# Performance work log

Measured on AMD Instinct MI355X. Metric: run time of the kernel, lower is better.

The kernel has to match this reference:

```python
import jax, jax.numpy as jnp
import numpy as np

B, T_IMG, H, W_ = 8, 64, 112, 112
T_Q, QDIM, D, NH, HD = 4096, 242, 512, 8, 64
MAX_KV = 512
NUM_CLASSES = 1296
F_IN = 3 * H * W_


def _ln(x, g, b, eps=1e-5):
    m = x.mean(-1, keepdims=True)
    v = ((x - m) ** 2).mean(-1, keepdims=True)
    return (x - m) * jax.lax.rsqrt(v + eps) * g + b


def _pool_mean(x, lengths, max_kv):
    # x: (B, T, D); per-row stride s = ceil(L / max_kv); pooled[j] = mean of window of size s
    # (zero-padded past L, divided by s), matching torch _pool_variable_1d(mode='mean').
    Bx, T, Dx = x.shape
    s = jnp.maximum((lengths + max_kv - 1) // max_kv, 1)          # (B,)
    S = -(-T // max_kv)                                            # static max stride
    j = jnp.arange(max_kv)
    i = jnp.arange(S)
    idx = j[None, :, None] * s[:, None, None] + i[None, None, :]   # (B, max_kv, S)
    valid = (i[None, None, :] < s[:, None, None]) & (idx < lengths[:, None, None])
    gi = jnp.minimum(idx, T - 1).reshape(Bx, -1)[:, :, None]       # (B, max_kv*S, 1)
    g = jnp.take_along_axis(x, gi, axis=1).reshape(Bx, max_kv, S, Dx)
    pooled = (g * valid[..., None].astype(x.dtype)).sum(2) / s[:, None, None].astype(x.dtype)
    new_len = (lengths + s - 1) // s                               # ceil(L/s) <= max_kv
    pad_mask = jnp.arange(max_kv)[None, :] >= new_len[:, None]     # True = PAD
    pooled = jnp.where(pad_mask[..., None], jnp.zeros((), x.dtype), pooled)
    return pooled, new_len, pad_mask


def setup_inputs() -> dict:
    key = jax.random.key(0)
    ks = jax.random.split(key, 20)
    sc = lambda n: np.float32(1.0 / np.sqrt(n))
    d = {}
    d["images"] = jax.random.normal(ks[0], (B, T_IMG, 3, H, W_), jnp.float32)
    d["qgrids"] = jax.random.normal(ks[1], (B, T_Q, QDIM), jnp.float32)
    d["keypoints"] = jax.random.normal(ks[2], (B, T_IMG, QDIM), jnp.float32)
    d["qgrid_lengths"] = jax.random.randint(ks[3], (B,), 512, T_Q + 1)
    d["W_img"] = jax.random.normal(ks[4], (F_IN, D), jnp.float32) * sc(F_IN)
    d["b_img"] = jnp.zeros((D,), jnp.float32)
    d["W_kp"] = jax.random.normal(ks[5], (QDIM, D), jnp.float32) * sc(QDIM)
    d["b_kp"] = jnp.zeros((D,), jnp.float32)
    d["g_kp"] = jnp.ones((D,), jnp.float32)
    d["bt_kp"] = jnp.zeros((D,), jnp.float32)
    d["W_qp"] = jax.random.normal(ks[6], (QDIM, D), jnp.float32) * sc(QDIM)
    d["b_qp"] = jnp.zeros((D,), jnp.float32)
    d["g_qln"] = jnp.ones((D,), jnp.float32)
    d["bt_qln"] = jnp.zeros((D,), jnp.float32)
    d["Wq"] = jax.random.normal(ks[7], (D, D), jnp.float32) * sc(D)
    d["bq"] = jnp.zeros((D,), jnp.float32)
    d["Wk"] = jax.random.normal(ks[8], (D, D), jnp.float32) * sc(D)
    d["bk"] = jnp.zeros((D,), jnp.float32)
    d["Wv"] = jax.random.normal(ks[9], (D, D), jnp.float32) * sc(D)
    d["bv"] = jnp.zeros((D,), jnp.float32)
    d["Wo"] = jax.random.normal(ks[10], (D, D), jnp.float32) * sc(D)
    d["bo"] = jnp.zeros((D,), jnp.float32)
    d["g_attn"] = jnp.ones((D,), jnp.float32)
    d["bt_attn"] = jnp.zeros((D,), jnp.float32)
    d["W_ctc"] = jax.random.normal(ks[11], (2 * D, NUM_CLASSES), jnp.float32) * sc(2 * D)
    d["b_ctc"] = jnp.zeros((NUM_CLASSES,), jnp.float32)
    return d


def reference(images, qgrids, keypoints, qgrid_lengths, W_img, b_img, W_kp, b_kp,
              g_kp, bt_kp, W_qp, b_qp, g_qln, bt_qln, Wq, bq, Wk, bk, Wv, bv,
              Wo, bo, g_attn, bt_attn, W_ctc, b_ctc):
    Bx, T = images.shape[:2]
    # image encoder stub: per-frame flatten -> linear -> (B, T, D)
    img_feat = images.reshape(Bx, T, -1) @ W_img + b_img
    kp_feat = _ln(jax.nn.relu(keypoints @ W_kp + b_kp), g_kp, bt_kp)
    low = img_feat + kp_feat                                       # (B, T_img, D)
    # qgrid proj + LN, then ragged variable-stride mean pooling to <= MAX_KV tokens
    q_emb = _ln(qgrids @ W_qp + b_qp, g_qln, bt_qln)               # (B, T_q, D)
    q_emb, q_lens, pad = _pool_mean(q_emb, qgrid_lengths, MAX_KV)  # (B, MAX_KV, D)
    # cross attention: queries = low-freq frames, keys/values = pooled qgrid tokens
    q = (low @ Wq + bq).reshape(Bx, T, NH, HD)
    k = (q_emb @ Wk + bk).reshape(Bx, MAX_KV, NH, HD)
    v = (q_emb @ Wv + bv).reshape(Bx, MAX_KV, NH, HD)
    scores = jnp.einsum('bqhd,bkhd->bhqk', q, k) * (1.0 / np.sqrt(HD))
    scores = jnp.where(pad[:, None, None, :], jnp.asarray(-1e9, scores.dtype), scores)
    attn = jax.nn.softmax(scores, axis=-1)
    ctx = jnp.einsum('bhqk,bkhd->bqhd', attn, v).reshape(Bx, T, D)
    ctx = _ln(ctx @ Wo + bo, g_attn, bt_attn)
    fused = jnp.concatenate([low, ctx], axis=-1)                   # (B, T_img, 2D)
    return fused @ W_ctc + b_ctc                                   # (B, T_img, V)
```

## Files before the change

### kernel.cpp

```cpp
#include <hip/hip_runtime.h>
#include <hip/hip_bf16.h>

typedef __bf16 bf16x8 __attribute__((ext_vector_type(8)));
typedef __bf16 bf16x4 __attribute__((ext_vector_type(4)));
typedef float f32x4 __attribute__((ext_vector_type(4)));
typedef float f32x2 __attribute__((ext_vector_type(2)));

__device__ __forceinline__ f32x4 mfma16(bf16x8 a, bf16x8 b, f32x4 c) {
  return __builtin_amdgcn_mfma_f32_16x16x32_bf16(a, b, c, 0, 0, 0);
}

__device__ __forceinline__ bf16x8 cvt8(const float* f) {
  bf16x8 r;
#pragma unroll
  for (int i = 0; i < 8; ++i) r[i] = (__bf16)f[i];
  return r;
}

#define SYNC_LGKM() \
  asm volatile("s_waitcnt lgkmcnt(0)\n\ts_barrier" ::: "memory")

__device__ __forceinline__ void blockRed2(float& a, float& b, float* red) {
#pragma unroll
  for (int off = 1; off < 64; off <<= 1) {
    a += __shfl_xor(a, off, 64);
    b += __shfl_xor(b, off, 64);
  }
  const int w = threadIdx.x >> 6;
  if ((threadIdx.x & 63) == 0) { red[w] = a; red[4 + w] = b; }
  __syncthreads();
  a = red[0] + red[1] + red[2] + red[3];
  b = red[4] + red[5] + red[6] + red[7];
  __syncthreads();
}

#define IMG_K 37632
#define SPLITK 49
#define STEPS_PER 24

__global__ __launch_bounds__(512) void img_gemm_kernel(
    const float* __restrict__ A, const float* __restrict__ B,
    __bf16* __restrict__ partials) {
  __shared__ __bf16 As[2][128 * 40];
  __shared__ __bf16 Bs[2][128 * 40];
  const int t = threadIdx.x;
  const int lane = t & 63;
  const int w = t >> 6;
  const int wr = (w >> 2) * 64;
  const int wc = (w & 3) * 32;
  const int orig = blockIdx.x + (blockIdx.y << 2) + (blockIdx.z << 4);
  const int swz = (orig & 7) * 98 + (orig >> 3);
  const int m0 = ((swz >> 2) & 3) * 128;
  const int n0 = (swz & 3) * 128;
  const int zz = swz >> 4;
  const int step0 = zz * STEPS_PER;

  f32x4 acc[4][2];
#pragma unroll
  for (int i = 0; i < 4; ++i)
#pragma unroll
    for (int j = 0; j < 2; ++j) acc[i][j] = f32x4{0.f, 0.f, 0.f, 0.f};

  const int ar = t >> 2, ak = (t & 3) * 8;
  const int bn = t & 127, bk = (t >> 7) * 8;
  const int fr = lane & 15, fk = (lane >> 4) * 8;

  float r0a[8], r0b[8], r1a[8], r1b[8], r2a[8], r2b[8];
#define IMG_LOAD(AT, BT, K0)                                                \
  do {                                                                      \
    const float* asrc = A + (size_t)(m0 + ar) * IMG_K + (K0) + ak;          \
    f32x4 v0 = *reinterpret_cast<const f32x4*>(asrc);                       \
    f32x4 v1 = *reinterpret_cast<const f32x4*>(asrc + 4);                   \
    AT[0] = v0[0]; AT[1] = v0[1]; AT[2] = v0[2]; AT[3] = v0[3];             \
    AT[4] = v1[0]; AT[5] = v1[1]; AT[6] = v1[2]; AT[7] = v1[3];             \
    const float* bsrc = B + (size_t)((K0) + bk) * 512 + n0 + bn;            \
    _Pragma("unroll") for (int j = 0; j < 8; ++j) BT[j] =                   \
        bsrc[(size_t)j * 512];                                              \
  } while (0)
#define IMG_WRITE(BUF, AT, BT)                                              \
  do {                                                                      \
    *reinterpret_cast<bf16x8*>(&As[BUF][ar * 40 + ak]) = cvt8(AT);          \
    *reinterpret_cast<bf16x8*>(&Bs[BUF][bn * 40 + bk]) = cvt8(BT);          \
  } while (0)
#define IMG_MFMA(BUF)                                                       \
  do {                                                                      \
    bf16x8 af[4], bfr[2];                                                   \
    _Pragma("unroll") for (int i = 0; i < 4; ++i) af[i] =                   \
        *reinterpret_cast<const bf16x8*>(                                   \
            &As[BUF][(wr + i * 16 + fr) * 40 + fk]);                        \
    _Pragma("unroll") for (int j = 0; j < 2; ++j) bfr[j] =                  \
        *reinterpret_cast<const bf16x8*>(                                   \
            &Bs[BUF][(wc + j * 16 + fr) * 40 + fk]);                        \
    _Pragma("unroll") for (int i = 0; i < 4; ++i)                           \
        _Pragma("unroll") for (int j = 0; j < 2; ++j) acc[i][j] =           \
            mfma16(af[i], bfr[j], acc[i][j]);                               \
  } while (0)
#define IMG_STEP(S, BUF, WBUF, LA, LB, WA, WB)                              \
  do {                                                                      \
    if ((S) + 3 < STEPS_PER) IMG_LOAD(LA, LB, (step0 + (S) + 3) * 32);      \
    IMG_MFMA(BUF);                                                          \
    if ((S) + 1 < STEPS_PER) IMG_WRITE(WBUF, WA, WB);                       \
    SYNC_LGKM();                                                            \
  } while (0)

  IMG_LOAD(r0a, r0b, step0 * 32);
  IMG_WRITE(0, r0a, r0b);
  IMG_LOAD(r1a, r1b, (step0 + 1) * 32);
  IMG_LOAD(r2a, r2b, (step0 + 2) * 32);
  SYNC_LGKM();

  for (int s6 = 0; s6 < STEPS_PER; s6 += 6) {
    IMG_STEP(s6 + 0, 0, 1, r0a, r0b, r1a, r1b);
    IMG_STEP(s6 + 1, 1, 0, r1a, r1b, r2a, r2b);
    IMG_STEP(s6 + 2, 0, 1, r2a, r2b, r0a, r0b);
    IMG_STEP(s6 + 3, 1, 0, r0a, r0b, r1a, r1b);
    IMG_STEP(s6 + 4, 0, 1, r1a, r1b, r2a, r2b);
    IMG_STEP(s6 + 5, 1, 0, r2a, r2b, r0a, r0b);
  }
#undef IMG_LOAD
#undef IMG_WRITE
#undef IMG_MFMA
#undef IMG_STEP

  __bf16* P = partials + (size_t)zz * (512 * 512);
  const int rq = (lane >> 4) * 4;
#pragma unroll
  for (int i = 0; i < 4; ++i)
#pragma unroll
    for (int j = 0; j < 2; ++j)
#pragma unroll
      for (int r = 0; r < 4; ++r)
        P[(size_t)(m0 + wr + i * 16 + rq + r) * 512 + (n0 + wc + j * 16 + fr)] =
            (__bf16)acc[i][j][r];
}

__global__ __launch_bounds__(256) void reduce_add_kernel(
    const __bf16* __restrict__ partials, const float* __restrict__ b_img,
    float* __restrict__ low, __bf16* __restrict__ fusedbf) {
  const int idx = blockIdx.x * 256 + threadIdx.x;
  float acc = low[idx] + b_img[idx & 511];
#pragma unroll
  for (int z = 0; z < SPLITK; ++z)
    acc += (float)partials[(size_t)z * 262144 + idx];
  low[idx] = acc;
  fusedbf[(size_t)(idx >> 9) * 1024 + (idx & 511)] = (__bf16)acc;
}

__global__ __launch_bounds__(256) void prep3_kernel(
    const float* __restrict__ W_qp, __bf16* __restrict__ wtq,
    const float* __restrict__ W_kp, __bf16* __restrict__ wkp_t,
    const float* __restrict__ kp, __bf16* __restrict__ kpbf) {
  const int bid = blockIdx.x;
  const int t = threadIdx.x;
  if (bid < 512) {
    wtq[(size_t)bid * 256 + t] =
        (t < 242) ? (__bf16)W_qp[(size_t)t * 512 + bid] : (__bf16)0.f;
  } else if (bid < 1024) {
    const int c = bid - 512;
    wkp_t[(size_t)c * 256 + t] =
        (t < 242) ? (__bf16)W_kp[(size_t)t * 512 + c] : (__bf16)0.f;
  } else {
    const int r = bid - 1024;
    kpbf[(size_t)r * 256 + t] =
        (t < 242) ? (__bf16)kp[(size_t)r * 242 + t] : (__bf16)0.f;
  }
}

__global__ __launch_bounds__(256) void kp_gemm_kernel(
    const __bf16* __restrict__ A, const __bf16* __restrict__ Wt,
    const float* __restrict__ bias, float* __restrict__ C) {
  const int t = threadIdx.x, lane = t & 63, w = t >> 6;
  const int n0 = blockIdx.x * 16;
  const int m0 = blockIdx.y * 64 + w * 16;
  const int fr = lane & 15, fq = lane >> 4;
  const __bf16* arow = A + (size_t)(m0 + fr) * 256 + fq * 8;
  const __bf16* brow = Wt + (size_t)(n0 + fr) * 256 + fq * 8;
  f32x4 acc = f32x4{0.f, 0.f, 0.f, 0.f};
#pragma unroll
  for (int ks = 0; ks < 8; ++ks) {
    bf16x8 a = *reinterpret_cast<const bf16x8*>(arow + ks * 32);
    bf16x8 b = *reinterpret_cast<const bf16x8*>(brow + ks * 32);
    acc = mfma16(a, b, acc);
  }
  const int col = n0 + fr;
  const float bv = bias[col];
  const int r0 = m0 + fq * 4;
#pragma unroll
  for (int r = 0; r < 4; ++r)
    C[(size_t)(r0 + r) * 512 + col] = fmaxf(acc[r] + bv, 0.f);
}

__global__ __launch_bounds__(256) void ln_f32_kernel(
    const float* __restrict__ x, const float* __restrict__ g,
    const float* __restrict__ bt, float* __restrict__ y) {
  __shared__ float red[8];
  const int t = threadIdx.x;
  const size_t off = (size_t)blockIdx.x * 512;
  const float a = x[off + t], b2 = x[off + t + 256];
  float s = a + b2, sq = a * a + b2 * b2;
  blockRed2(s, sq, red);
  const float m = s * (1.f / 512.f);
  const float var = sq * (1.f / 512.f) - m * m;
  const float rs = rsqrtf(var + 1e-5f);
  y[off + t] = (a - m) * rs * g[t] + bt[t];
  y[off + t + 256] = (b2 - m) * rs * g[t + 256] + bt[t + 256];
}

__device__ __forceinline__ void wtrans_body(const float* __restrict__ W,
                                            __bf16* __restrict__ Wt, int NC,
                                            int NK, int bx, int by) {
  __shared__ float T[32][33];
  const int t = threadIdx.x;
  const int c0 = bx * 32;
  const int k0 = by * 32;
#pragma unroll
  for (int r = 0; r < 4; ++r) {
    const int idx = r * 256 + t;
    const int i = idx >> 5, j = idx & 31;
    const int c = c0 + j;
    T[i][j] = (c < NC) ? W[(size_t)(k0 + i) * NC + c] : 0.f;
  }
  __syncthreads();
#pragma unroll
  for (int r = 0; r < 4; ++r) {
    const int idx = r * 256 + t;
    const int i = idx >> 5, j = idx & 31;
    const int c = c0 + i;
    if (c < NC) Wt[(size_t)c * NK + k0 + j] = (__bf16)T[j][i];
  }
}

__global__ __launch_bounds__(256) void wtrans_kernel(
    const float* __restrict__ W, __bf16* __restrict__ Wt, int NC, int NK) {
  wtrans_body(W, Wt, NC, NK, blockIdx.x, blockIdx.y);
}

__global__ __launch_bounds__(256) void wtrans4_kernel(
    const float* __restrict__ W0, const float* __restrict__ W1,
    const float* __restrict__ W2, const float* __restrict__ W3,
    __bf16* __restrict__ T0, __bf16* __restrict__ T1,
    __bf16* __restrict__ T2, __bf16* __restrict__ T3) {
  const float* W = (blockIdx.z == 0) ? W0 : (blockIdx.z == 1) ? W1
                   : (blockIdx.z == 2) ? W2 : W3;
  __bf16* Wt = (blockIdx.z == 0) ? T0 : (blockIdx.z == 1) ? T1
               : (blockIdx.z == 2) ? T2 : T3;
  wtrans_body(W, Wt, 512, 512, blockIdx.x, blockIdx.y);
}

__global__ __launch_bounds__(512) void pool_mfma_kernel(
    const float* __restrict__ qgrids, const int* __restrict__ lens,
    const __bf16* __restrict__ Wt, const float* __restrict__ bias,
    const float* __restrict__ g, const float* __restrict__ bt,
    __bf16* __restrict__ pooled) {
  __shared__ float red[8][16][2];
  __shared__ float Arows[16][258];
  const int t = threadIdx.x, lane = t & 63, w = t >> 6;
  const int b = blockIdx.x >> 5;
  const int j0 = (blockIdx.x & 31) * 16;
  const int L = lens[b];
  int S = (L + 511) >> 9;
  if (S < 1) S = 1;
  const int new_len = (L + S - 1) / S;
  const float* qg_b = qgrids + (size_t)b * 4096 * 242;
  __bf16* pooled_b = pooled + (size_t)b * 512 * 512;

  const int fr = lane & 15;
  const int fq = lane >> 4;
  const int fkq = fq * 8;
  const int colbase = w * 64;

  float biasv[4], gv[4], btv[4];
#pragma unroll
  for (int nt = 0; nt < 4; ++nt) {
    const int col = colbase + nt * 16 + fr;
    biasv[nt] = bias[col];
    gv[nt] = g[col];
    btv[nt] = bt[col];
  }

  f32x4 pool[4];
#pragma unroll
  for (int nt = 0; nt < 4; ++nt) pool[nt] = f32x4{0.f, 0.f, 0.f, 0.f};

  {
    const int row = t >> 5, l32 = t & 31;
    if (l32 < 16) Arows[row][242 + l32] = 0.f;
  }

  for (int i = 0; i < S; ++i) {
    {
      const int row = t >> 5, l32 = t & 31;
      const int arow = (j0 + row) * S + i;
      const float* src = qg_b + (size_t)arow * 242;
#pragma unroll
      for (int c8 = 0; c8 < 4; ++c8) {
        const int c = (l32 + c8 * 32) * 2;
        if (c < 242) {
          f32x2 v = *reinterpret_cast<const f32x2*>(src + c);
          Arows[row][c] = v[0];
          Arows[row][c + 1] = v[1];
        }
      }
    }
    __syncthreads();
    f32x4 acc[4];
#pragma unroll
    for (int nt = 0; nt < 4; ++nt) acc[nt] = f32x4{0.f, 0.f, 0.f, 0.f};
#pragma unroll
    for (int ks = 0; ks < 8; ++ks) {
      bf16x8 af = cvt8(&Arows[fr][ks * 32 + fkq]);
      const __bf16* wt = Wt + ks * 32 + fkq;
#pragma unroll
      for (int nt = 0; nt < 4; ++nt) {
        bf16x8 bfv = *reinterpret_cast<const bf16x8*>(
            wt + (size_t)(colbase + nt * 16 + fr) * 256);
        acc[nt] = mfma16(af, bfv, acc[nt]);
      }
    }
    float s[4] = {0.f, 0.f, 0.f, 0.f}, sq[4] = {0.f, 0.f, 0.f, 0.f};
#pragma unroll
    for (int nt = 0; nt < 4; ++nt) {
#pragma unroll
      for (int r = 0; r < 4; ++r) {
        const float v = acc[nt][r] + biasv[nt];
        acc[nt][r] = v;
        s[r] += v;
        sq[r] += v * v;
      }
    }
#pragma unroll
    for (int off = 1; off < 16; off <<= 1) {
#pragma unroll
      for (int r = 0; r < 4; ++r) {
        s[r] += __shfl_xor(s[r], off, 64);
        sq[r] += __shfl_xor(sq[r], off, 64);
      }
    }
    if (fr == 0) {
#pragma unroll
      for (int r = 0; r < 4; ++r) {
        red[w][fq * 4 + r][0] = s[r];
        red[w][fq * 4 + r][1] = sq[r];
      }
    }
    __syncthreads();
    float mean[4], rsig[4];
#pragma unroll
    for (int r = 0; r < 4; ++r) {
      const int p = fq * 4 + r;
      float ss = 0.f, qq = 0.f;
#pragma unroll
      for (int ww = 0; ww < 8; ++ww) {
        ss += red[ww][p][0];
        qq += red[ww][p][1];
      }
      const float m = ss * (1.f / 512.f);
      mean[r] = m;
      rsig[r] = rsqrtf(qq * (1.f / 512.f) - m * m + 1e-5f);
    }
    __syncthreads();
#pragma unroll
    for (int r = 0; r < 4; ++r) {
      const int srow = (j0 + fq * 4 + r) * S + i;
      const bool ok = srow < L;
#pragma unroll
      for (int nt = 0; nt < 4; ++nt) {
        const float nv = (acc[nt][r] - mean[r]) * rsig[r] * gv[nt] + btv[nt];
        pool[nt][r] += ok ? nv : 0.f;
      }
    }
  }
  const float inv = 1.f / (float)S;
#pragma unroll
  for (int r = 0; r < 4; ++r) {
    const int j = j0 + fq * 4 + r;
    const bool ok = j < new_len;
#pragma unroll
    for (int nt = 0; nt < 4; ++nt)
      pooled_b[(size_t)j * 512 + colbase + nt * 16 + fr] =
          (__bf16)(ok ? pool[nt][r] * inv : 0.f);
  }
}

template <typename OutT>
__global__ __launch_bounds__(256) void reg_gemm512_kernel(
    const __bf16* __restrict__ A, int lda, const __bf16* __restrict__ Wt,
    const float* __restrict__ bias, OutT* __restrict__ C, int ldc) {
  const int t = threadIdx.x, lane = t & 63, w = t >> 6;
  const int n0 = blockIdx.x * 16;
  const int m0 = blockIdx.y * 64 + w * 16;
  const int fr = lane & 15, fq = lane >> 4;
  const __bf16* arow = A + (size_t)(m0 + fr) * lda + fq * 8;
  const __bf16* brow = Wt + (size_t)(n0 + fr) * 512 + fq * 8;
  f32x4 acc = f32x4{0.f, 0.f, 0.f, 0.f};
#pragma unroll
  for (int ks = 0; ks < 16; ++ks) {
    bf16x8 a = *reinterpret_cast<const bf16x8*>(arow + ks * 32);
    bf16x8 b = *reinterpret_cast<const bf16x8*>(brow + ks * 32);
    acc = mfma16(a, b, acc);
  }
  const int col = n0 + fr;
  const float bv = bias[col];
  const int r0 = m0 + fq * 4;
#pragma unroll
  for (int r = 0; r < 4; ++r)
    C[(size_t)(r0 + r) * ldc + col] = (OutT)(acc[r] + bv);
}

__global__ __launch_bounds__(256) void kv_reg_gemm_kernel(
    const __bf16* __restrict__ A, const __bf16* __restrict__ wk_t,
    const float* __restrict__ bk, const __bf16* __restrict__ wv_t,
    const float* __restrict__ bv, __bf16* __restrict__ kout,
    __bf16* __restrict__ vout) {
  const __bf16* Wt = blockIdx.z ? wv_t : wk_t;
  const float* bias = blockIdx.z ? bv : bk;
  __bf16* C = blockIdx.z ? vout : kout;
  const int t = threadIdx.x, lane = t & 63, w = t >> 6;
  const int n0 = blockIdx.x * 16;
  const int m0 = blockIdx.y * 64 + w * 16;
  const int fr = lane & 15, fq = lane >> 4;
  const __bf16* arow = A + (size_t)(m0 + fr) * 512 + fq * 8;
  const __bf16* brow = Wt + (size_t)(n0 + fr) * 512 + fq * 8;
  f32x4 acc = f32x4{0.f, 0.f, 0.f, 0.f};
#pragma unroll
  for (int ks = 0; ks < 16; ++ks) {
    bf16x8 a = *reinterpret_cast<const bf16x8*>(arow + ks * 32);
    bf16x8 b = *reinterpret_cast<const bf16x8*>(brow + ks * 32);
    acc = mfma16(a, b, acc);
  }
  const int col = n0 + fr;
  const float bvv = bias[col];
  const int r0 = m0 + fq * 4;
#pragma unroll
  for (int r = 0; r < 4; ++r)
    C[(size_t)(r0 + r) * 512 + col] = (__bf16)(acc[r] + bvv);
}

__global__ __launch_bounds__(256) void ctc_gemm_kernel(
    const __bf16* __restrict__ A, const __bf16* __restrict__ Wt,
    const float* __restrict__ bias, float* __restrict__ out) {
  const int t = threadIdx.x, lane = t & 63, w = t >> 6;
  const int n0 = blockIdx.x * 16;
  const int m0 = blockIdx.y * 64 + w * 16;
  const int fr = lane & 15, fq = lane >> 4;
  const __bf16* arow = A + (size_t)(m0 + fr) * 1024 + fq * 8;
  const __bf16* brow = Wt + (size_t)(n0 + fr) * 1024 + fq * 8;
  f32x4 acc = f32x4{0.f, 0.f, 0.f, 0.f};
#pragma unroll
  for (int ks = 0; ks < 32; ++ks) {
    bf16x8 a = *reinterpret_cast<const bf16x8*>(arow + ks * 32);
    bf16x8 b = *reinterpret_cast<const bf16x8*>(brow + ks * 32);
    acc = mfma16(a, b, acc);
  }
  const int col = n0 + fr;
  const float bv = bias[col];
  const int r0 = m0 + fq * 4;
#pragma unroll
  for (int r = 0; r < 4; ++r)
    out[(size_t)(r0 + r) * 1296 + col] = acc[r] + bv;
}

__global__ __launch_bounds__(256) void attn_fused_kernel(
    const __bf16* __restrict__ q, const __bf16* __restrict__ k,
    const __bf16* __restrict__ v, const int* __restrict__ lens,
    __bf16* __restrict__ ctx) {
  __shared__ __bf16 Qs[64 * 72];
  __shared__ __bf16 Ps[64 * 520];
  __shared__ __bf16 KVs[64 * 520];
  const int t = threadIdx.x, lane = t & 63, w = t >> 6;
  const int bh = blockIdx.x, b = bh >> 3, h = bh & 7;
  const int L = lens[b];
  const int sdiv = (L + 511) >> 9;
  const int new_len = (L + sdiv - 1) / sdiv;
  const size_t qbase = (size_t)b * 64 * 512 + h * 64;
  const size_t kbase = (size_t)b * 512 * 512 + h * 64;
  const size_t vbase = kbase;
  const int fr = lane & 15, fkq = (lane >> 4) * 8;

#pragma unroll
  for (int rep = 0; rep < 4; ++rep) {
    const int gidx = rep * 256 + t;
    const int row = gidx >> 4, c = (gidx & 15) * 4;
    *reinterpret_cast<bf16x4*>(&Qs[row * 72 + c]) =
        *reinterpret_cast<const bf16x4*>(&q[qbase + (size_t)row * 512 + c]);
  }
  f32x4 acc[32];
#pragma unroll
  for (int nt = 0; nt < 32; ++nt) acc[nt] = f32x4{0.f, 0.f, 0.f, 0.f};
  for (int ks = 0; ks < 2; ++ks) {
    const int k0 = ks * 32;
#pragma unroll
    for (int rep = 0; rep < 16; ++rep) {
      const int gidx = rep * 256 + t;
      const int row = gidx >> 3, c = (gidx & 7) * 4;
      *reinterpret_cast<bf16x4*>(&KVs[row * 40 + c]) =
          *reinterpret_cast<const bf16x4*>(&k[kbase + (size_t)row * 512 + k0 + c]);
    }
    __syncthreads();
    const bf16x8 af =
        *reinterpret_cast<const bf16x8*>(&Qs[(w * 16 + fr) * 72 + k0 + fkq]);
#pragma unroll
    for (int nt = 0; nt < 32; ++nt) {
      bf16x8 bf = *reinterpret_cast<const bf16x8*>(&KVs[(nt * 16 + fr) * 40 + fkq]);
      acc[nt] = mfma16(af, bf, acc[nt]);
    }
    __syncthreads();
  }
  const float scale = 0.125f;
#pragma unroll
  for (int r = 0; r < 4; ++r) {
    float mx = -3.0e38f;
#pragma unroll
    for (int nt = 0; nt < 32; ++nt) {
      const int col = nt * 16 + fr;
      const float sv = acc[nt][r] * scale;
      if (col < new_len) mx = fmaxf(mx, sv);
    }
#pragma unroll
    for (int off = 1; off < 16; off <<= 1) mx = fmaxf(mx, __shfl_xor(mx, off, 64));
    float sum = 0.f;
#pragma unroll
    for (int nt = 0; nt < 32; ++nt) {
      const int col = nt * 16 + fr;
      const float e = (col < new_len) ? __expf(acc[nt][r] * scale - mx) : 0.f;
      acc[nt][r] = e;
      sum += e;
    }
#pragma unroll
    for (int off = 1; off < 16; off <<= 1) sum += __shfl_xor(sum, off, 64);
    const float inv = 1.f / sum;
    const int row = w * 16 + ((lane >> 4) << 2) + r;
#pragma unroll
    for (int nt = 0; nt < 32; ++nt)
      Ps[row * 520 + nt * 16 + fr] = (__bf16)(acc[nt][r] * inv);
  }
  __syncthreads();
  {
    const int d = t & 63;
    const int kc = (t >> 6) * 128;
    const int sw = (d & 7) << 3;
#pragma unroll
    for (int j8 = 0; j8 < 16; ++j8) {
      const int kv0 = kc + j8 * 8;
      bf16x8 tmp;
#pragma unroll
      for (int jj = 0; jj < 8; ++jj)
        tmp[jj] = v[vbase + (size_t)(kv0 + jj) * 512 + d];
      *reinterpret_cast<bf16x8*>(&KVs[d * 520 + (kv0 ^ sw)]) = tmp;
    }
  }
  __syncthreads();
  f32x4 acc2[4];
#pragma unroll
  for (int nt = 0; nt < 4; ++nt) acc2[nt] = f32x4{0.f, 0.f, 0.f, 0.f};
  const int swr = (fr & 7) << 3;
#pragma unroll
  for (int s = 0; s < 16; ++s) {
    const int k0 = s * 32;
    const bf16x8 af =
        *reinterpret_cast<const bf16x8*>(&Ps[(w * 16 + fr) * 520 + k0 + fkq]);
#pragma unroll
    for (int nt = 0; nt < 4; ++nt) {
      bf16x8 bf = *reinterpret_cast<const bf16x8*>(
          &KVs[(nt * 16 + fr) * 520 + ((k0 + fkq) ^ swr)]);
      acc2[nt] = mfma16(af, bf, acc2[nt]);
    }
  }
  const int rq = (lane >> 4) * 4;
  const size_t cbase = (size_t)b * 64 * 512 + h * 64;
#pragma unroll
  for (int nt = 0; nt < 4; ++nt)
#pragma unroll
    for (int r = 0; r < 4; ++r)
      ctx[cbase + (size_t)(w * 16 + rq + r) * 512 + nt * 16 + fr] =
          (__bf16)acc2[nt][r];
}

__global__ __launch_bounds__(256) void ln_bf16_kernel(
    const float* __restrict__ x, const float* __restrict__ g,
    const float* __restrict__ bt, __bf16* __restrict__ ybf) {
  __shared__ float red[8];
  const int t = threadIdx.x;
  const size_t off = (size_t)blockIdx.x * 512;
  const float a = x[off + t], b2 = x[off + t + 256];
  float s = a + b2, sq = a * a + b2 * b2;
  blockRed2(s, sq, red);
  const float m = s * (1.f / 512.f);
  const float var = sq * (1.f / 512.f) - m * m;
  const float rs = rsqrtf(var + 1e-5f);
  __bf16* yrow = ybf + (size_t)blockIdx.x * 1024;
  yrow[t] = (__bf16)((a - m) * rs * g[t] + bt[t]);
  yrow[t + 256] = (__bf16)((b2 - m) * rs * g[t + 256] + bt[t + 256]);
}

extern "C" void kernel_launch(void* const* d_in, const int* in_sizes, int n_in,
                              void* d_out, int out_size, void* d_ws,
                              size_t ws_size, hipStream_t stream) {
  const float* images = (const float*)d_in[0];
  const float* qgrids = (const float*)d_in[1];
  const float* keypoints = (const float*)d_in[2];
  const int* qlens = (const int*)d_in[3];
  const float* W_img = (const float*)d_in[4];
  const float* b_img = (const float*)d_in[5];
  const float* W_kp = (const float*)d_in[6];
  const float* b_kp = (const float*)d_in[7];
  const float* g_kp = (const float*)d_in[8];
  const float* bt_kp = (const float*)d_in[9];
  const float* W_qp = (const float*)d_in[10];
  const float* b_qp = (const float*)d_in[11];
  const float* g_qln = (const float*)d_in[12];
  const float* bt_qln = (const float*)d_in[13];
  const float* Wq = (const float*)d_in[14];
  const float* bq = (const float*)d_in[15];
  const float* Wk = (const float*)d_in[16];
  const float* bk = (const float*)d_in[17];
  const float* Wv = (const float*)d_in[18];
  const float* bv = (const float*)d_in[19];
  const float* Wo = (const float*)d_in[20];
  const float* bo = (const float*)d_in[21];
  const float* g_attn = (const float*)d_in[22];
  const float* bt_attn = (const float*)d_in[23];
  const float* W_ctc = (const float*)d_in[24];
  const float* b_ctc = (const float*)d_in[25];
  float* out = (float*)d_out;

  const size_t MB = 1u << 20;
  const size_t KB = 1u << 10;
  if (ws_size < 35 * MB + 512 * KB) return;
  char* ws = (char*)d_ws;
  float* low = (float*)(ws);
  __bf16* qbuf = (__bf16*)(ws + 1 * MB);
  __bf16* wtq = (__bf16*)(ws + 2 * MB);
  float* ctxo = (float*)(ws + 2 * MB);
  __bf16* fusedbf = (__bf16*)(ws + 3 * MB);
  __bf16* partials = (__bf16*)(ws + 4 * MB);
  __bf16* pooled = (__bf16*)(ws + 4 * MB);
  __bf16* kbuf = (__bf16*)(ws + 12 * MB);
  __bf16* vbuf = (__bf16*)(ws + 16 * MB);
  __bf16* ctxbf = (__bf16*)(ws + 28 * MB);
  __bf16* wtc = (__bf16*)(ws + 29 * MB);
  __bf16* wq_t = (__bf16*)(ws + 32 * MB);
  __bf16* wk_t = (__bf16*)(ws + 32 * MB + 512 * KB);
  __bf16* wv_t = (__bf16*)(ws + 33 * MB);
  __bf16* wo_t = (__bf16*)(ws + 33 * MB + 512 * KB);
  __bf16* kpbf = (__bf16*)(ws + 34 * MB);
  __bf16* wkp_t = (__bf16*)(ws + 34 * MB + 256 * KB);
  float* kptmp = (float*)(ws + 34 * MB + 512 * KB);

  prep3_kernel<<<1536, 256, 0, stream>>>(W_qp, wtq, W_kp, wkp_t, keypoints,
                                         kpbf);
  wtrans4_kernel<<<dim3(16, 16, 4), 256, 0, stream>>>(Wq, Wk, Wv, Wo, wq_t,
                                                      wk_t, wv_t, wo_t);
  wtrans_kernel<<<dim3(41, 32), 256, 0, stream>>>(W_ctc, wtc, 1296, 1024);
  img_gemm_kernel<<<dim3(4, 4, SPLITK), 512, 0, stream>>>(images, W_img, partials);
  kp_gemm_kernel<<<dim3(32, 8), 256, 0, stream>>>(kpbf, wkp_t, b_kp, kptmp);
  ln_f32_kernel<<<512, 256, 0, stream>>>(kptmp, g_kp, bt_kp, low);
  reduce_add_kernel<<<1024, 256, 0, stream>>>(partials, b_img, low, fusedbf);
  pool_mfma_kernel<<<256, 512, 0, stream>>>(qgrids, qlens, wtq, b_qp, g_qln,
                                            bt_qln, pooled);
  kv_reg_gemm_kernel<<<dim3(32, 64, 2), 256, 0, stream>>>(pooled, wk_t, bk,
                                                          wv_t, bv, kbuf, vbuf);
  reg_gemm512_kernel<__bf16><<<dim3(32, 8), 256, 0, stream>>>(
      fusedbf, 1024, wq_t, bq, qbuf, 512);
  attn_fused_kernel<<<64, 256, 0, stream>>>(qbuf, kbuf, vbuf, qlens, ctxbf);
  reg_gemm512_kernel<float><<<dim3(32, 8), 256, 0, stream>>>(
      ctxbf, 512, wo_t, bo, ctxo, 512);
  ln_bf16_kernel<<<512, 256, 0, stream>>>(ctxo, g_attn, bt_attn, fusedbf + 512);
  ctc_gemm_kernel<<<dim3(81, 8), 256, 0, stream>>>(fusedbf, wtc, b_ctc, out);
}
```

Measured before the change: 224.2 us.

## Merge pool, image split-K GEMM and keypoint GEMM into one launch

The qgrid pooling, image split-K GEMM and keypoint GEMM run as different block ranges of a single phase1 kernel that shares a union of shared memory. The independent stages can then overlap on the GPU and two launch gaps disappear. The keypoint LayerNorm is also fused with the split-K reduction into one kernel, which drops a float round-trip through the low buffer. The workspace is re-laid out so partials and K/V buffers share space. Risks are heterogeneous blocks raising register pressure for the pool path at 512 threads and load imbalance between block types.

After: 204.2 us, median of 3. -8.9%, faster.

```diff
diff --git a/kernel.cpp b/kernel.cpp
--- a/kernel.cpp
+++ b/kernel.cpp
@@ -38,17 +38,14 @@
 #define SPLITK 49
 #define STEPS_PER 24
 
-__global__ __launch_bounds__(512) void img_gemm_kernel(
-    const float* __restrict__ A, const float* __restrict__ B,
-    __bf16* __restrict__ partials) {
-  __shared__ __bf16 As[2][128 * 40];
-  __shared__ __bf16 Bs[2][128 * 40];
+__device__ __forceinline__ void img_body(
+    int orig, const float* __restrict__ A, const float* __restrict__ B,
+    __bf16* __restrict__ partials, __bf16 (*As)[5120], __bf16 (*Bs)[5120]) {
   const int t = threadIdx.x;
   const int lane = t & 63;
   const int w = t >> 6;
   const int wr = (w >> 2) * 64;
   const int wc = (w & 3) * 32;
-  const int orig = blockIdx.x + (blockIdx.y << 2) + (blockIdx.z << 4);
   const int swz = (orig & 7) * 98 + (orig >> 3);
   const int m0 = ((swz >> 2) & 3) * 128;
   const int n0 = (swz & 3) * 128;
@@ -134,16 +131,216 @@
             (__bf16)acc[i][j][r];
 }
 
-__global__ __launch_bounds__(256) void reduce_add_kernel(
-    const __bf16* __restrict__ partials, const float* __restrict__ b_img,
-    float* __restrict__ low, __bf16* __restrict__ fusedbf) {
-  const int idx = blockIdx.x * 256 + threadIdx.x;
-  float acc = low[idx] + b_img[idx & 511];
-#pragma unroll
-  for (int z = 0; z < SPLITK; ++z)
-    acc += (float)partials[(size_t)z * 262144 + idx];
-  low[idx] = acc;
-  fusedbf[(size_t)(idx >> 9) * 1024 + (idx & 511)] = (__bf16)acc;
+__device__ __forceinline__ void pool_body(
+    int pbid, const float* __restrict__ qgrids, const int* __restrict__ lens,
+    const __bf16* __restrict__ Wt, const float* __restrict__ bias,
+    const float* __restrict__ g, const float* __restrict__ bt,
+    __bf16* __restrict__ pooled, float (*red)[16][2], float (*Arows)[258]) {
+  const int t = threadIdx.x, lane = t & 63, w = t >> 6;
+  const int b = pbid >> 5;
+  const int j0 = (pbid & 31) * 16;
+  const int L = lens[b];
+  int S = (L + 511) >> 9;
+  if (S < 1) S = 1;
+  const int new_len = (L + S - 1) / S;
+  const float* qg_b = qgrids + (size_t)b * 4096 * 242;
+  __bf16* pooled_b = pooled + (size_t)b * 512 * 512;
+
+  const int fr = lane & 15;
+  const int fq = lane >> 4;
+  const int fkq = fq * 8;
+  const int colbase = w * 64;
+
+  float biasv[4], gv[4], btv[4];
+#pragma unroll
+  for (int nt = 0; nt < 4; ++nt) {
+    const int col = colbase + nt * 16 + fr;
+    biasv[nt] = bias[col];
+    gv[nt] = g[col];
+    btv[nt] = bt[col];
+  }
+
+  f32x4 pool[4];
+#pragma unroll
+  for (int nt = 0; nt < 4; ++nt) pool[nt] = f32x4{0.f, 0.f, 0.f, 0.f};
+
+  {
+    const int row = t >> 5, l32 = t & 31;
+    if (l32 < 16) Arows[row][242 + l32] = 0.f;
+  }
+
+  for (int i = 0; i < S; ++i) {
+    {
+      const int row = t >> 5, l32 = t & 31;
+      const int arow = (j0 + row) * S + i;
+      const float* src = qg_b + (size_t)arow * 242;
+#pragma unroll
+      for (int c8 = 0; c8 < 4; ++c8) {
+        const int c = (l32 + c8 * 32) * 2;
+        if (c < 242) {
+          f32x2 v = *reinterpret_cast<const f32x2*>(src + c);
+          Arows[row][c] = v[0];
+          Arows[row][c + 1] = v[1];
+        }
+      }
+    }
+    __syncthreads();
+    f32x4 acc[4];
+#pragma unroll
+    for (int nt = 0; nt < 4; ++nt) acc[nt] = f32x4{0.f, 0.f, 0.f, 0.f};
+#pragma unroll
+    for (int ks = 0; ks < 8; ++ks) {
+      bf16x8 af = cvt8(&Arows[fr][ks * 32 + fkq]);
+      const __bf16* wt = Wt + ks * 32 + fkq;
+#pragma unroll
+      for (int nt = 0; nt < 4; ++nt) {
+        bf16x8 bfv = *reinterpret_cast<const bf16x8*>(
+            wt + (size_t)(colbase + nt * 16 + fr) * 256);
+        acc[nt] = mfma16(af, bfv, acc[nt]);
+      }
+    }
+    float s[4] = {0.f, 0.f, 0.f, 0.f}, sq[4] = {0.f, 0.f, 0.f, 0.f};
+#pragma unroll
+    for (int nt = 0; nt < 4; ++nt) {
+#pragma unroll
+      for (int r = 0; r < 4; ++r) {
+        const float v = acc[nt][r] + biasv[nt];
+        acc[nt][r] = v;
+        s[r] += v;
+        sq[r] += v * v;
+      }
+    }
+#pragma unroll
+    for (int off = 1; off < 16; off <<= 1) {
+#pragma unroll
+      for (int r = 0; r < 4; ++r) {
+        s[r] += __shfl_xor(s[r], off, 64);
+        sq[r] += __shfl_xor(sq[r], off, 64);
+      }
+    }
+    if (fr == 0) {
+#pragma unroll
+      for (int r = 0; r < 4; ++r) {
+        red[w][fq * 4 + r][0] = s[r];
+        red[w][fq * 4 + r][1] = sq[r];
+      }
+    }
+    __syncthreads();
+    float mean[4], rsig[4];
+#pragma unroll
+    for (int r = 0; r < 4; ++r) {
+      const int p = fq * 4 + r;
+      float ss = 0.f, qq = 0.f;
+#pragma unroll
+      for (int ww = 0; ww < 8; ++ww) {
+        ss += red[ww][p][0];
+        qq += red[ww][p][1];
+      }
+      const float m = ss * (1.f / 512.f);
+      mean[r] = m;
+      rsig[r] = rsqrtf(qq * (1.f / 512.f) - m * m + 1e-5f);
+    }
+    __syncthreads();
+#pragma unroll
+    for (int r = 0; r < 4; ++r) {
+      const int srow = (j0 + fq * 4 + r) * S + i;
+      const bool ok = srow < L;
+#pragma unroll
+      for (int nt = 0; nt < 4; ++nt) {
+        const float nv = (acc[nt][r] - mean[r]) * rsig[r] * gv[nt] + btv[nt];
+        pool[nt][r] += ok ? nv : 0.f;
+      }
+    }
+  }
+  const float inv = 1.f / (float)S;
+#pragma unroll
+  for (int r = 0; r < 4; ++r) {
+    const int j = j0 + fq * 4 + r;
+    const bool ok = j < new_len;
+#pragma unroll
+    for (int nt = 0; nt < 4; ++nt)
+      pooled_b[(size_t)j * 512 + colbase + nt * 16 + fr] =
+          (__bf16)(ok ? pool[nt][r] * inv : 0.f);
+  }
+}
+
+__device__ __forceinline__ void kp_body(
+    int kpbid, const __bf16* __restrict__ A, const __bf16* __restrict__ Wt,
+    const float* __restrict__ bias, float* __restrict__ C) {
+  const int t = threadIdx.x, lane = t & 63, w = t >> 6;
+  const int n0 = (kpbid & 31) * 16;
+  const int m0 = (kpbid >> 5) * 128 + w * 16;
+  const int fr = lane & 15, fq = lane >> 4;
+  const __bf16* arow = A + (size_t)(m0 + fr) * 256 + fq * 8;
+  const __bf16* brow = Wt + (size_t)(n0 + fr) * 256 + fq * 8;
+  f32x4 acc = f32x4{0.f, 0.f, 0.f, 0.f};
+#pragma unroll
+  for (int ks = 0; ks < 8; ++ks) {
+    bf16x8 a = *reinterpret_cast<const bf16x8*>(arow + ks * 32);
+    bf16x8 b = *reinterpret_cast<const bf16x8*>(brow + ks * 32);
+    acc = mfma16(a, b, acc);
+  }
+  const int col = n0 + fr;
+  const float bv = bias[col];
+  const int r0 = m0 + fq * 4;
+#pragma unroll
+  for (int r = 0; r < 4; ++r)
+    C[(size_t)(r0 + r) * 512 + col] = fmaxf(acc[r] + bv, 0.f);
+}
+
+__global__ __launch_bounds__(512) void phase1_kernel(
+    const float* __restrict__ images, const float* __restrict__ W_img,
+    __bf16* __restrict__ partials, const float* __restrict__ qgrids,
+    const int* __restrict__ lens, const __bf16* __restrict__ wtq,
+    const float* __restrict__ b_qp, const float* __restrict__ g_qln,
+    const float* __restrict__ bt_qln, __bf16* __restrict__ pooled,
+    const __bf16* __restrict__ kpbf, const __bf16* __restrict__ wkp_t,
+    const float* __restrict__ b_kp, float* __restrict__ kptmp) {
+  __shared__ union {
+    struct {
+      __bf16 As[2][5120];
+      __bf16 Bs[2][5120];
+    } img;
+    struct {
+      float red[8][16][2];
+      float Arows[16][258];
+    } pool;
+  } sm;
+  const int bid = blockIdx.x;
+  if (bid < 256) {
+    pool_body(bid, qgrids, lens, wtq, b_qp, g_qln, bt_qln, pooled,
+              sm.pool.red, sm.pool.Arows);
+  } else if (bid < 1040) {
+    img_body(bid - 256, images, W_img, partials, sm.img.As, sm.img.Bs);
+  } else {
+    kp_body(bid - 1040, kpbf, wkp_t, b_kp, kptmp);
+  }
+}
+
+__global__ __launch_bounds__(256) void reduce_ln_kernel(
+    const float* __restrict__ kptmp, const float* __restrict__ g,
+    const float* __restrict__ bt, const __bf16* __restrict__ partials,
+    const float* __restrict__ b_img, __bf16* __restrict__ fusedbf) {
+  __shared__ float red[8];
+  const int t = threadIdx.x;
+  const int row = blockIdx.x;
+  const size_t off = (size_t)row * 512;
+  const float a = kptmp[off + t], b2 = kptmp[off + t + 256];
+  float s = a + b2, sq = a * a + b2 * b2;
+  blockRed2(s, sq, red);
+  const float m = s * (1.f / 512.f);
+  const float var = sq * (1.f / 512.f) - m * m;
+  const float rs = rsqrtf(var + 1e-5f);
+  float acc0 = (a - m) * rs * g[t] + bt[t] + b_img[t];
+  float acc1 = (b2 - m) * rs * g[t + 256] + bt[t + 256] + b_img[t + 256];
+#pragma unroll
+  for (int z = 0; z < SPLITK; ++z) {
+    acc0 += (float)partials[(size_t)z * 262144 + off + t];
+    acc1 += (float)partials[(size_t)z * 262144 + off + t + 256];
+  }
+  __bf16* dst = fusedbf + (size_t)row * 1024;
+  dst[t] = (__bf16)acc0;
+  dst[t + 256] = (__bf16)acc1;
 }
 
 __global__ __launch_bounds__(256) void prep3_kernel(
@@ -166,46 +363,6 @@
   }
 }
 
-__global__ __launch_bounds__(256) void kp_gemm_kernel(
-    const __bf16* __restrict__ A, const __bf16* __restrict__ Wt,
-    const float* __restrict__ bias, float* __restrict__ C) {
-  const int t = threadIdx.x, lane = t & 63, w = t >> 6;
-  const int n0 = blockIdx.x * 16;
-  const int m0 = blockIdx.y * 64 + w * 16;
-  const int fr = lane & 15, fq = lane >> 4;
-  const __bf16* arow = A + (size_t)(m0 + fr) * 256 + fq * 8;
-  const __bf16* brow = Wt + (size_t)(n0 + fr) * 256 + fq * 8;
-  f32x4 acc = f32x4{0.f, 0.f, 0.f, 0.f};
-#pragma unroll
-  for (int ks = 0; ks < 8; ++ks) {
-    bf16x8 a = *reinterpret_cast<const bf16x8*>(arow + ks * 32);
-    bf16x8 b = *reinterpret_cast<const bf16x8*>(brow + ks * 32);
-    acc = mfma16(a, b, acc);
-  }
-  const int col = n0 + fr;
-  const float bv = bias[col];
-  const int r0 = m0 + fq * 4;
-#pragma unroll
-  for (int r = 0; r < 4; ++r)
-    C[(size_t)(r0 + r) * 512 + col] = fmaxf(acc[r] + bv, 0.f);
-}
-
-__global__ __launch_bounds__(256) void ln_f32_kernel(
-    const float* __restrict__ x, const float* __restrict__ g,
-    const float* __restrict__ bt, float* __restrict__ y) {
-  __shared__ float red[8];
-  const int t = threadIdx.x;
-  const size_t off = (size_t)blockIdx.x * 512;
-  const float a = x[off + t], b2 = x[off + t + 256];
-  float s = a + b2, sq = a * a + b2 * b2;
-  blockRed2(s, sq, red);
-  const float m = s * (1.f / 512.f);
-  const float var = sq * (1.f / 512.f) - m * m;
-  const float rs = rsqrtf(var + 1e-5f);
-  y[off + t] = (a - m) * rs * g[t] + bt[t];
-  y[off + t + 256] = (b2 - m) * rs * g[t + 256] + bt[t + 256];
-}
-
 __device__ __forceinline__ void wtrans_body(const float* __restrict__ W,
                                             __bf16* __restrict__ Wt, int NC,
                                             int NK, int bx, int by) {
@@ -245,141 +402,6 @@
   __bf16* Wt = (blockIdx.z == 0) ? T0 : (blockIdx.z == 1) ? T1
                : (blockIdx.z == 2) ? T2 : T3;
   wtrans_body(W, Wt, 512, 512, blockIdx.x, blockIdx.y);
-}
-
-__global__ __launch_bounds__(512) void pool_mfma_kernel(
-    const float* __restrict__ qgrids, const int* __restrict__ lens,
-    const __bf16* __restrict__ Wt, const float* __restrict__ bias,
-    const float* __restrict__ g, const float* __restrict__ bt,
-    __bf16* __restrict__ pooled) {
-  __shared__ float red[8][16][2];
-  __shared__ float Arows[16][258];
-  const int t = threadIdx.x, lane = t & 63, w = t >> 6;
-  const int b = blockIdx.x >> 5;
-  const int j0 = (blockIdx.x & 31) * 16;
-  const int L = lens[b];
-  int S = (L + 511) >> 9;
-  if (S < 1) S = 1;
-  const int new_len = (L + S - 1) / S;
-  const float* qg_b = qgrids + (size_t)b * 4096 * 242;
-  __bf16* pooled_b = pooled + (size_t)b * 512 * 512;
-
-  const int fr = lane & 15;
-  const int fq = lane >> 4;
-  const int fkq = fq * 8;
-  const int colbase = w * 64;
-
-  float biasv[4], gv[4], btv[4];
-#pragma unroll
-  for (int nt = 0; nt < 4; ++nt) {
-    const int col = colbase + nt * 16 + fr;
-    biasv[nt] = bias[col];
-    gv[nt] = g[col];
-    btv[nt] = bt[col];
-  }
-
-  f32x4 pool[4];
-#pragma unroll
-  for (int nt = 0; nt < 4; ++nt) pool[nt] = f32x4{0.f, 0.f, 0.f, 0.f};
-
-  {
-    const int row = t >> 5, l32 = t & 31;
-    if (l32 < 16) Arows[row][242 + l32] = 0.f;
-  }
-
-  for (int i = 0; i < S; ++i) {
-    {
-      const int row = t >> 5, l32 = t & 31;
-      const int arow = (j0 + row) * S + i;
-      const float* src = qg_b + (size_t)arow * 242;
-#pragma unroll
-      for (int c8 = 0; c8 < 4; ++c8) {
-        const int c = (l32 + c8 * 32) * 2;
-        if (c < 242) {
-          f32x2 v = *reinterpret_cast<const f32x2*>(src + c);
-          Arows[row][c] = v[0];
-          Arows[row][c + 1] = v[1];
-        }
-      }
-    }
-    __syncthreads();
-    f32x4 acc[4];
-#pragma unroll
-    for (int nt = 0; nt < 4; ++nt) acc[nt] = f32x4{0.f, 0.f, 0.f, 0.f};
-#pragma unroll
-    for (int ks = 0; ks < 8; ++ks) {
-      bf16x8 af = cvt8(&Arows[fr][ks * 32 + fkq]);
-      const __bf16* wt = Wt + ks * 32 + fkq;
-#pragma unroll
-      for (int nt = 0; nt < 4; ++nt) {
-        bf16x8 bfv = *reinterpret_cast<const bf16x8*>(
-            wt + (size_t)(colbase + nt * 16 + fr) * 256);
-        acc[nt] = mfma16(af, bfv, acc[nt]);
-      }
-    }
-    float s[4] = {0.f, 0.f, 0.f, 0.f}, sq[4] = {0.f, 0.f, 0.f, 0.f};
-#pragma unroll
-    for (int nt = 0; nt < 4; ++nt) {
-#pragma unroll
-      for (int r = 0; r < 4; ++r) {
-        const float v = acc[nt][r] + biasv[nt];
-        acc[nt][r] = v;
-        s[r] += v;
-        sq[r] += v * v;
-      }
-    }
-#pragma unroll
-    for (int off = 1; off < 16; off <<= 1) {
-#pragma unroll
-      for (int r = 0; r < 4; ++r) {
-        s[r] += __shfl_xor(s[r], off, 64);
-        sq[r] += __shfl_xor(sq[r], off, 64);
-      }
-    }
-    if (fr == 0) {
-#pragma unroll
-      for (int r = 0; r < 4; ++r) {
-        red[w][fq * 4 + r][0] = s[r];
-        red[w][fq * 4 + r][1] = sq[r];
-      }
-    }
-    __syncthreads();
-    float mean[4], rsig[4];
-#pragma unroll
-    for (int r = 0; r < 4; ++r) {
-      const int p = fq * 4 + r;
-      float ss = 0.f, qq = 0.f;
-#pragma unroll
-      for (int ww = 0; ww < 8; ++ww) {
-        ss += red[ww][p][0];
-        qq += red[ww][p][1];
-      }
-      const float m = ss * (1.f / 512.f);
-      mean[r] = m;
-      rsig[r] = rsqrtf(qq * (1.f / 512.f) - m * m + 1e-5f);
-    }
-    __syncthreads();
-#pragma unroll
-    for (int r = 0; r < 4; ++r) {
-      const int srow = (j0 + fq * 4 + r) * S + i;
-      const bool ok = srow < L;
-#pragma unroll
-      for (int nt = 0; nt < 4; ++nt) {
-        const float nv = (acc[nt][r] - mean[r]) * rsig[r] * gv[nt] + btv[nt];
-        pool[nt][r] += ok ? nv : 0.f;
-      }
-    }
-  }
-  const float inv = 1.f / (float)S;
-#pragma unroll
-  for (int r = 0; r < 4; ++r) {
-    const int j = j0 + fq * 4 + r;
-    const bool ok = j < new_len;
-#pragma unroll
-    for (int nt = 0; nt < 4; ++nt)
-      pooled_b[(size_t)j * 512 + colbase + nt * 16 + fr] =
-          (__bf16)(ok ? pool[nt][r] * inv : 0.f);
-  }
 }
 
 template <typename OutT>
@@ -626,38 +648,36 @@
 
   const size_t MB = 1u << 20;
   const size_t KB = 1u << 10;
-  if (ws_size < 35 * MB + 512 * KB) return;
+  if (ws_size < 35 * MB) return;
   char* ws = (char*)d_ws;
-  float* low = (float*)(ws);
+  float* kptmp = (float*)(ws);
   __bf16* qbuf = (__bf16*)(ws + 1 * MB);
+  __bf16* ctxbf = (__bf16*)(ws + 1 * MB + 512 * KB);
   __bf16* wtq = (__bf16*)(ws + 2 * MB);
   float* ctxo = (float*)(ws + 2 * MB);
   __bf16* fusedbf = (__bf16*)(ws + 3 * MB);
-  __bf16* partials = (__bf16*)(ws + 4 * MB);
   __bf16* pooled = (__bf16*)(ws + 4 * MB);
-  __bf16* kbuf = (__bf16*)(ws + 12 * MB);
-  __bf16* vbuf = (__bf16*)(ws + 16 * MB);
-  __bf16* ctxbf = (__bf16*)(ws + 28 * MB);
-  __bf16* wtc = (__bf16*)(ws + 29 * MB);
-  __bf16* wq_t = (__bf16*)(ws + 32 * MB);
-  __bf16* wk_t = (__bf16*)(ws + 32 * MB + 512 * KB);
-  __bf16* wv_t = (__bf16*)(ws + 33 * MB);
-  __bf16* wo_t = (__bf16*)(ws + 33 * MB + 512 * KB);
-  __bf16* kpbf = (__bf16*)(ws + 34 * MB);
-  __bf16* wkp_t = (__bf16*)(ws + 34 * MB + 256 * KB);
-  float* kptmp = (float*)(ws + 34 * MB + 512 * KB);
+  __bf16* partials = (__bf16*)(ws + 8 * MB);
+  __bf16* kbuf = (__bf16*)(ws + 8 * MB);
+  __bf16* vbuf = (__bf16*)(ws + 12 * MB);
+  __bf16* wtc = (__bf16*)(ws + 16 * MB);
+  __bf16* wq_t = (__bf16*)(ws + 32 * MB + 512 * KB);
+  __bf16* wk_t = (__bf16*)(ws + 33 * MB);
+  __bf16* wv_t = (__bf16*)(ws + 33 * MB + 512 * KB);
+  __bf16* wo_t = (__bf16*)(ws + 34 * MB);
+  __bf16* kpbf = (__bf16*)(ws + 34 * MB + 512 * KB);
+  __bf16* wkp_t = (__bf16*)(ws + 34 * MB + 768 * KB);
 
   prep3_kernel<<<1536, 256, 0, stream>>>(W_qp, wtq, W_kp, wkp_t, keypoints,
                                          kpbf);
   wtrans4_kernel<<<dim3(16, 16, 4), 256, 0, stream>>>(Wq, Wk, Wv, Wo, wq_t,
                                                       wk_t, wv_t, wo_t);
+  phase1_kernel<<<1168, 512, 0, stream>>>(images, W_img, partials, qgrids,
+                                          qlens, wtq, b_qp, g_qln, bt_qln,
+                                          pooled, kpbf, wkp_t, b_kp, kptmp);
+  reduce_ln_kernel<<<512, 256, 0, stream>>>(kptmp, g_kp, bt_kp, partials,
+                                            b_img, fusedbf);
   wtrans_kernel<<<dim3(41, 32), 256, 0, stream>>>(W_ctc, wtc, 1296, 1024);
-  img_gemm_kernel<<<dim3(4, 4, SPLITK), 512, 0, stream>>>(images, W_img, partials);
-  kp_gemm_kernel<<<dim3(32, 8), 256, 0, stream>>>(kpbf, wkp_t, b_kp, kptmp);
-  ln_f32_kernel<<<512, 256, 0, stream>>>(kptmp, g_kp, bt_kp, low);
-  reduce_add_kernel<<<1024, 256, 0, stream>>>(partials, b_img, low, fusedbf);
-  pool_mfma_kernel<<<256, 512, 0, stream>>>(qgrids, qlens, wtq, b_qp, g_qln,
-                                            bt_qln, pooled);
   kv_reg_gemm_kernel<<<dim3(32, 64, 2), 256, 0, stream>>>(pooled, wk_t, bk,
                                                           wv_t, bv, kbuf, vbuf);
   reg_gemm512_kernel<__bf16><<<dim3(32, 8), 256, 0, stream>>>(
```
